# Optimization experiments

Hardware: AMD Instinct MI355X
Metric: run time of the kernel (lower is better)

## Reference

```python
import jax, jax.numpy as jnp
import numpy as np

B, N, D, H = 2, 512, 128, 8
DK = D // H

def setup_inputs() -> dict:
    key = jax.random.key(0)
    ks = jax.random.split(key, 7)
    s = lambda fan_in: 1.0 / np.sqrt(fan_in)
    return {
        "n": jax.random.normal(ks[0], (B, N, D), dtype=jnp.float32),
        "e": jax.random.normal(ks[1], (B, N, N, D), dtype=jnp.float32),
        "W_qkv": jax.random.normal(ks[2], (D, 3 * D), dtype=jnp.float32) * s(D),
        "O_n": jax.random.normal(ks[3], (D, D), dtype=jnp.float32) * s(D),
        "W_g": jax.random.normal(ks[4], (D, H), dtype=jnp.float32) * s(D),
        "W_e": jax.random.normal(ks[5], (D, H), dtype=jnp.float32) * s(D),
        "O_e": jax.random.normal(ks[6], (H, D), dtype=jnp.float32) * s(H),
    }

def reference(n, e, W_qkv, O_n, W_g, W_e, O_e):
    b, nn_, d = n.shape
    # QKV projection -> [B, H, N, DK] each
    qkv = (n @ W_qkv).reshape(b, nn_, 3, H, DK)
    qkv = jnp.transpose(qkv, (2, 0, 3, 1, 4))
    Q, K, V = qkv[0], qkv[1], qkv[2]
    # Edge bias and gate: [B, H, N, N]
    E = jnp.einsum('bnmd,dh->bhnm', e, W_e)
    G = jax.nn.sigmoid(jnp.einsum('bnmd,dh->bhnm', e, W_g))
    dyn_cent = jnp.log1p(G.sum(-1))  # [B, H, N]
    # Attention scores with clamp + edge bias
    A_raw = jnp.einsum('bhnd,bhmd->bhnm', Q, K) * (DK ** -0.5)
    A_raw = jnp.clip(A_raw, -5.0, 5.0)
    _E = A_raw + E
    A = jax.nn.softmax(_E, axis=-1)
    # Weighted values, rescaled by dynamic centrality
    _V = jnp.einsum('bhnm,bhmd->bhnd', A, V) * dyn_cent[..., None]
    n_out = jnp.transpose(_V, (0, 2, 1, 3)).reshape(b, nn_, d) @ O_n
    e_out = jnp.einsum('bhnm,hd->bnmd', _E, O_e)
    return n_out, e_out
```

## Files before the change

kernel.cpp:

```cpp
#include <hip/hip_runtime.h>
#include <math.h>

#define BB 2
#define NN 512
#define DD 128
#define HH 8
#define DKK 16
#define TR 128
#define NT (NN / TR)

typedef __attribute__((ext_vector_type(8))) short short8;
typedef __attribute__((ext_vector_type(4))) float f32x4;

__device__ __forceinline__ float dot4(float4 a, float4 b) {
    return a.x*b.x + a.y*b.y + a.z*b.z + a.w*b.w;
}
__device__ __forceinline__ unsigned pk_bf16(float a, float b) {
    unsigned ua = __float_as_uint(a), ub = __float_as_uint(b);
    ua = (ua + 0x7FFFu + ((ua >> 16) & 1u)) >> 16;
    ub = (ub + 0x7FFFu + ((ub >> 16) & 1u)) >> 16;
    return ua | (ub << 16);
}

__global__ __launch_bounds__(128)
void qkv_kernel(const float* __restrict__ n_in,
                const float* __restrict__ W_qkv,
                const float* __restrict__ W_g,
                const float* __restrict__ W_e,
                float* __restrict__ Qw, float* __restrict__ Kw,
                float* __restrict__ Vw, float* __restrict__ WegT)
{
    const int bid = blockIdx.x;
    if (bid >= BB * NN) {
        const int col = bid - BB * NN;
        const int t = threadIdx.x;
        WegT[col * DD + t] = (col < 8) ? W_e[t * HH + col]
                                       : W_g[t * HH + (col - 8)];
        return;
    }
    __shared__ float nrow[DD];
    const int bn = bid;
    const int b  = bn >> 9;
    const int nr = bn & 511;
    const int t  = threadIdx.x;
    nrow[t] = n_in[(size_t)bn * DD + t];
    __syncthreads();
    const int h = t >> 4, dk = t & 15;
    const size_t dst = ((size_t)(b * HH + h) * NN + nr) * DKK + dk;
    float accq = 0.f, acck = 0.f, accv = 0.f;
    #pragma unroll 8
    for (int d = 0; d < DD; ++d) {
        const float nv = nrow[d];
        const float* wr = W_qkv + (size_t)d * 3 * DD;
        accq += nv * wr[t];
        acck += nv * wr[t + 128];
        accv += nv * wr[t + 256];
    }
    Qw[dst] = accq;
    Kw[dst] = acck;
    Vw[dst] = accv;
}

__global__ __launch_bounds__(256)
void qk_kernel(const float* __restrict__ Qw,
               const float* __restrict__ Kw,
               float* __restrict__ QKc)
{
    __shared__ __align__(16) float4 Kl[NN * 4];
    __shared__ __align__(16) float4 Ql[32 * 4];

    const int bid = blockIdx.x;
    const int qt  = bid & 15;
    const int h   = (bid >> 4) & 7;
    const int b   = bid >> 7;
    const int t   = threadIdx.x;

    const float4* __restrict__ kb =
        (const float4*)Kw + ((size_t)(b * HH + h) * NN) * 4;
    #pragma unroll
    for (int j = 0; j < 8; ++j) Kl[j * 256 + t] = kb[j * 256 + t];
    if (t < 128)
        Ql[t] = ((const float4*)Qw)[((size_t)(b * HH + h) * NN + qt * 32) * 4 + t];
    __syncthreads();

    const int qr = t >> 3;
    const int mq = t & 7;
    const float4 q0 = Ql[qr * 4 + 0];
    const float4 q1 = Ql[qr * 4 + 1];
    const float4 q2 = Ql[qr * 4 + 2];
    const float4 q3 = Ql[qr * 4 + 3];

    float4* __restrict__ out4 =
        (float4*)QKc + (((size_t)(b * NN + qt * 32 + qr) * HH + h) * NN) / 4;

    #pragma unroll 1
    for (int c = 0; c < 16; ++c) {
        float4 r;
        float* rp = (float*)&r;
        #pragma unroll
        for (int i = 0; i < 4; ++i) {
            const int m = mq * 64 + c * 4 + i;
            float s = dot4(q0, Kl[m*4+0]) + dot4(q1, Kl[m*4+1])
                    + dot4(q2, Kl[m*4+2]) + dot4(q3, Kl[m*4+3]);
            s *= 0.25f;
            rp[i] = fminf(5.f, fmaxf(-5.f, s));
        }
        out4[mq * 16 + c] = r;
    }
}

__global__ __attribute__((amdgpu_flat_work_group_size(512, 512),
                          amdgpu_waves_per_eu(2, 4)))
void eg_kernel(const float* __restrict__ e,
               const float* __restrict__ WegT,
               const float* __restrict__ O_e,
               const float* __restrict__ QKc,
               const float* __restrict__ Vw,
               const float* __restrict__ O_n,
               float* __restrict__ n_out,
               float* __restrict__ e_out)
{
    __shared__ __align__(16) uint4 ebuf4[TR * 16];
    __shared__ __align__(16) float ET[HH * NN];
    __shared__ float Gred[64];
    __shared__ float dc[HH];
    __shared__ __align__(16) float vout[DD];

    const int t    = threadIdx.x;
    const int bn   = blockIdx.x;
    const int b    = bn >> 9;
    const int wq   = t >> 6;
    const int lane = t & 63;
    const int c    = lane & 15;
    const int mq   = lane >> 4;
    const int c4o  = t & 31;
    const int mr0  = t >> 5;

    const float4* __restrict__ e4    = (const float4*)e + (size_t)bn * NN * 32;
    const float4* __restrict__ WegT4 = (const float4*)WegT;

    short8 wB[4];
    #pragma unroll
    for (int kb = 0; kb < 4; ++kb) {
        const float4 wa = WegT4[c * 32 + kb * 8 + mq * 2];
        const float4 wb = WegT4[c * 32 + kb * 8 + mq * 2 + 1];
        uint4 u;
        u.x = pk_bf16(wa.x, wa.y); u.y = pk_bf16(wa.z, wa.w);
        u.z = pk_bf16(wb.x, wb.y); u.w = pk_bf16(wb.z, wb.w);
        wB[kb] = *(short8*)&u;
    }

    float4 pa0, pa1, pa2, pa3, pb0, pb1, pb2, pb3;

    #define STAGE_LOAD(tile)                                                  \
    {                                                                         \
        const float4* __restrict__ sp = e4 + (size_t)(tile) * 4096 + 2 * t;   \
        pa0 = sp[0];    pb0 = sp[1];                                          \
        pa1 = sp[1024]; pb1 = sp[1025];                                       \
        pa2 = sp[2048]; pb2 = sp[2049];                                       \
        pa3 = sp[3072]; pb3 = sp[3073];                                       \
    }
    #define STAGE_WRITE(P, A, B)                                              \
    {                                                                         \
        const int ms = (P) * 32 + (t >> 4), ck = t & 15;                      \
        uint4 u;                                                              \
        u.x = pk_bf16(A.x, A.y); u.y = pk_bf16(A.z, A.w);                     \
        u.z = pk_bf16(B.x, B.y); u.w = pk_bf16(B.z, B.w);                     \
        ebuf4[ms * 16 + (ck ^ (ms & 15))] = u;                                \
    }
    #define STAGE_WRITE_ALL()                                                 \
    {                                                                         \
        STAGE_WRITE(0, pa0, pb0); STAGE_WRITE(1, pa1, pb1);                   \
        STAGE_WRITE(2, pa2, pb2); STAGE_WRITE(3, pa3, pb3);                   \
    }

    float ga0 = 0.f, ga1 = 0.f, ga2 = 0.f, ga3 = 0.f;

    STAGE_LOAD(0);
    STAGE_WRITE_ALL();
    asm volatile("s_waitcnt lgkmcnt(0)" ::: "memory");
    __builtin_amdgcn_s_barrier();

    #pragma unroll
    for (int tt = 0; tt < NT; ++tt) {
        float4 qkv4 = {0.f, 0.f, 0.f, 0.f};
        if (c < 8)
            qkv4 = *(const float4*)(QKc + ((size_t)bn * HH + c) * NN
                                    + tt * TR + wq * 16 + mq * 4);
        if (tt + 1 < NT) STAGE_LOAD(tt + 1);

        const int mrow = wq * 16 + c;
        f32x4 acc = {0.f, 0.f, 0.f, 0.f};
        #pragma unroll
        for (int kb = 0; kb < 4; ++kb) {
            const int ck = kb * 4 + mq;
            uint4 av = ebuf4[mrow * 16 + (ck ^ (mrow & 15))];
            acc = __builtin_amdgcn_mfma_f32_16x16x32_bf16(
                      *(short8*)&av, wB[kb], acc, 0, 0, 0);
        }

        const int mloc = tt * TR + wq * 16 + mq * 4;
        if (c < 8) {
            ET[c * NN + mloc + 0] = acc[0] + qkv4.x;
            ET[c * NN + mloc + 1] = acc[1] + qkv4.y;
            ET[c * NN + mloc + 2] = acc[2] + qkv4.z;
            ET[c * NN + mloc + 3] = acc[3] + qkv4.w;
        } else {
            ga0 += 1.f / (1.f + __expf(-acc[0]));
            ga1 += 1.f / (1.f + __expf(-acc[1]));
            ga2 += 1.f / (1.f + __expf(-acc[2]));
            ga3 += 1.f / (1.f + __expf(-acc[3]));
        }
        asm volatile("s_waitcnt lgkmcnt(0)" ::: "memory");
        __builtin_amdgcn_s_barrier();

        if (tt + 1 < NT) {
            STAGE_WRITE_ALL();
            asm volatile("s_waitcnt lgkmcnt(0)" ::: "memory");
            __builtin_amdgcn_s_barrier();
        }
    }

    if (c >= 8) {
        float s = ga0 + ga1 + ga2 + ga3;
        s += __shfl_xor(s, 16, 64);
        s += __shfl_xor(s, 32, 64);
        if (lane < 16) Gred[wq * 8 + (c - 8)] = s;
    }
    __syncthreads();
    if (t < 8) {
        float s = 0.f;
        #pragma unroll
        for (int w = 0; w < 8; ++w) s += Gred[w * 8 + t];
        dc[t] = log1pf(s);
    }
    __syncthreads();

    {
        float4 oe[8];
        #pragma unroll
        for (int h = 0; h < 8; ++h)
            oe[h] = ((const float4*)O_e)[h * 32 + c4o];
        float4* __restrict__ out4 = (float4*)e_out + (size_t)bn * NN * 32;
        #pragma unroll 4
        for (int it = 0; it < 32; ++it) {
            const int m = mr0 + it * 16;
            float4 rr{0.f, 0.f, 0.f, 0.f};
            #pragma unroll
            for (int h = 0; h < 8; ++h) {
                const float ev = ET[h * NN + m];
                rr.x += ev * oe[h].x;
                rr.y += ev * oe[h].y;
                rr.z += ev * oe[h].z;
                rr.w += ev * oe[h].w;
            }
            out4[m * 32 + c4o] = rr;
        }
    }

    {
        const int h = wq;
        float vals[8];
        float rmax = -1e30f;
        #pragma unroll
        for (int k = 0; k < 8; ++k) {
            vals[k] = ET[h * NN + k * 64 + lane];
            rmax = fmaxf(rmax, vals[k]);
        }
        #pragma unroll
        for (int off = 32; off >= 1; off >>= 1)
            rmax = fmaxf(rmax, __shfl_xor(rmax, off, 64));
        float sum = 0.f;
        #pragma unroll
        for (int k = 0; k < 8; ++k) sum += __expf(vals[k] - rmax);
        #pragma unroll
        for (int off = 32; off >= 1; off >>= 1)
            sum += __shfl_xor(sum, off, 64);
        const float factor = dc[h] / sum;

        const int ddx = lane & 15, mg = lane >> 4;
        const float* __restrict__ vb = Vw + ((size_t)(b * HH + h) * NN) * DKK;
        float av = 0.f;
        #pragma unroll 4
        for (int m = mg; m < NN; m += 4) {
            const float p = __expf(ET[h * NN + m] - rmax);
            av += p * vb[m * DKK + ddx];
        }
        av += __shfl_xor(av, 16, 64);
        av += __shfl_xor(av, 32, 64);
        if (mg == 0) vout[h * DKK + ddx] = av * factor;
    }
    __syncthreads();

    if (t < DD) {
        float a3 = 0.f;
        #pragma unroll 4
        for (int d = 0; d < DD; ++d) a3 += vout[d] * O_n[d * DD + t];
        n_out[(size_t)bn * DD + t] = a3;
    }
    #undef STAGE_LOAD
    #undef STAGE_WRITE
    #undef STAGE_WRITE_ALL
}

extern "C" void kernel_launch(void* const* d_in, const int* in_sizes, int n_in,
                              void* d_out, int out_size, void* d_ws, size_t ws_size,
                              hipStream_t stream)
{
    const float* n_ptr = (const float*)d_in[0];
    const float* e     = (const float*)d_in[1];
    const float* W_qkv = (const float*)d_in[2];
    const float* O_n   = (const float*)d_in[3];
    const float* W_g   = (const float*)d_in[4];
    const float* W_e   = (const float*)d_in[5];
    const float* O_e   = (const float*)d_in[6];

    float* n_out = (float*)d_out;
    float* e_out = n_out + (size_t)BB * NN * DD;

    float* Qw   = (float*)d_ws;
    float* Kw   = Qw + (size_t)BB * HH * NN * DKK;
    float* Vw   = Kw + (size_t)BB * HH * NN * DKK;
    float* QKc  = Vw + (size_t)BB * HH * NN * DKK;
    float* WegT = QKc + (size_t)BB * HH * NN * NN;

    qkv_kernel<<<BB * NN + 16, 128, 0, stream>>>(n_ptr, W_qkv, W_g, W_e,
                                                 Qw, Kw, Vw, WegT);
    qk_kernel<<<BB * HH * 16, 256, 0, stream>>>(Qw, Kw, QKc);
    eg_kernel<<<BB * NN, 512, 0, stream>>>(e, WegT, O_e, QKc, Vw, O_n,
                                           n_out, e_out);
}
```

Baseline: 173.0 us.

## Fuse QK score computation into edge kernel, drop QKc intermediate buffer

Removes the separate qk_kernel and its 8 MB global QKc scratch buffer, which was written and then re-read by the edge kernel. Each eg_kernel block now computes its own row of clamped Q·K scores per head directly from global Q and K (K reads hit L2) into shared memory before the MFMA loop, which then accumulates the edge bias onto them in place. The ET stride is padded to 516 to reduce bank conflicts. In exchange, every block re-reads the full K for its batch and does the dot products redundantly with scalar FMAs.

```diff
diff --git a/kernel.cpp b/kernel.cpp
--- a/kernel.cpp
+++ b/kernel.cpp
@@ -8,6 +8,7 @@
 #define DKK 16
 #define TR 128
 #define NT (NN / TR)
+#define ETS 516
 
 typedef __attribute__((ext_vector_type(8))) short short8;
 typedef __attribute__((ext_vector_type(4))) float f32x4;
@@ -61,67 +62,20 @@
     Vw[dst] = accv;
 }
 
-__global__ __launch_bounds__(256)
-void qk_kernel(const float* __restrict__ Qw,
-               const float* __restrict__ Kw,
-               float* __restrict__ QKc)
-{
-    __shared__ __align__(16) float4 Kl[NN * 4];
-    __shared__ __align__(16) float4 Ql[32 * 4];
-
-    const int bid = blockIdx.x;
-    const int qt  = bid & 15;
-    const int h   = (bid >> 4) & 7;
-    const int b   = bid >> 7;
-    const int t   = threadIdx.x;
-
-    const float4* __restrict__ kb =
-        (const float4*)Kw + ((size_t)(b * HH + h) * NN) * 4;
-    #pragma unroll
-    for (int j = 0; j < 8; ++j) Kl[j * 256 + t] = kb[j * 256 + t];
-    if (t < 128)
-        Ql[t] = ((const float4*)Qw)[((size_t)(b * HH + h) * NN + qt * 32) * 4 + t];
-    __syncthreads();
-
-    const int qr = t >> 3;
-    const int mq = t & 7;
-    const float4 q0 = Ql[qr * 4 + 0];
-    const float4 q1 = Ql[qr * 4 + 1];
-    const float4 q2 = Ql[qr * 4 + 2];
-    const float4 q3 = Ql[qr * 4 + 3];
-
-    float4* __restrict__ out4 =
-        (float4*)QKc + (((size_t)(b * NN + qt * 32 + qr) * HH + h) * NN) / 4;
-
-    #pragma unroll 1
-    for (int c = 0; c < 16; ++c) {
-        float4 r;
-        float* rp = (float*)&r;
-        #pragma unroll
-        for (int i = 0; i < 4; ++i) {
-            const int m = mq * 64 + c * 4 + i;
-            float s = dot4(q0, Kl[m*4+0]) + dot4(q1, Kl[m*4+1])
-                    + dot4(q2, Kl[m*4+2]) + dot4(q3, Kl[m*4+3]);
-            s *= 0.25f;
-            rp[i] = fminf(5.f, fmaxf(-5.f, s));
-        }
-        out4[mq * 16 + c] = r;
-    }
-}
-
 __global__ __attribute__((amdgpu_flat_work_group_size(512, 512),
                           amdgpu_waves_per_eu(2, 4)))
 void eg_kernel(const float* __restrict__ e,
                const float* __restrict__ WegT,
                const float* __restrict__ O_e,
-               const float* __restrict__ QKc,
+               const float* __restrict__ Qw,
+               const float* __restrict__ Kw,
                const float* __restrict__ Vw,
                const float* __restrict__ O_n,
                float* __restrict__ n_out,
                float* __restrict__ e_out)
 {
     __shared__ __align__(16) uint4 ebuf4[TR * 16];
-    __shared__ __align__(16) float ET[HH * NN];
+    __shared__ __align__(16) float ET[HH * ETS];
     __shared__ float Gred[64];
     __shared__ float dc[HH];
     __shared__ __align__(16) float vout[DD];
@@ -129,6 +83,7 @@
     const int t    = threadIdx.x;
     const int bn   = blockIdx.x;
     const int b    = bn >> 9;
+    const int nr   = bn & 511;
     const int wq   = t >> 6;
     const int lane = t & 63;
     const int c    = lane & 15;
@@ -177,16 +132,30 @@
     float ga0 = 0.f, ga1 = 0.f, ga2 = 0.f, ga3 = 0.f;
 
     STAGE_LOAD(0);
+
+    {
+        const int h = wq;
+        const float4* __restrict__ qp =
+            (const float4*)(Qw + ((size_t)(b * HH + h) * NN + nr) * DKK);
+        const float4 q0 = qp[0], q1 = qp[1], q2 = qp[2], q3 = qp[3];
+        const float4* __restrict__ kb =
+            (const float4*)(Kw + ((size_t)(b * HH + h) * NN) * DKK);
+        #pragma unroll
+        for (int k = 0; k < 8; ++k) {
+            const int m = k * 64 + lane;
+            float s = dot4(q0, kb[m * 4 + 0]) + dot4(q1, kb[m * 4 + 1])
+                    + dot4(q2, kb[m * 4 + 2]) + dot4(q3, kb[m * 4 + 3]);
+            s *= 0.25f;
+            ET[h * ETS + m] = fminf(5.f, fmaxf(-5.f, s));
+        }
+    }
+
     STAGE_WRITE_ALL();
     asm volatile("s_waitcnt lgkmcnt(0)" ::: "memory");
     __builtin_amdgcn_s_barrier();
 
     #pragma unroll
     for (int tt = 0; tt < NT; ++tt) {
-        float4 qkv4 = {0.f, 0.f, 0.f, 0.f};
-        if (c < 8)
-            qkv4 = *(const float4*)(QKc + ((size_t)bn * HH + c) * NN
-                                    + tt * TR + wq * 16 + mq * 4);
         if (tt + 1 < NT) STAGE_LOAD(tt + 1);
 
         const int mrow = wq * 16 + c;
@@ -201,10 +170,10 @@
 
         const int mloc = tt * TR + wq * 16 + mq * 4;
         if (c < 8) {
-            ET[c * NN + mloc + 0] = acc[0] + qkv4.x;
-            ET[c * NN + mloc + 1] = acc[1] + qkv4.y;
-            ET[c * NN + mloc + 2] = acc[2] + qkv4.z;
-            ET[c * NN + mloc + 3] = acc[3] + qkv4.w;
+            float4 prev = *(float4*)&ET[c * ETS + mloc];
+            prev.x += acc[0]; prev.y += acc[1];
+            prev.z += acc[2]; prev.w += acc[3];
+            *(float4*)&ET[c * ETS + mloc] = prev;
         } else {
             ga0 += 1.f / (1.f + __expf(-acc[0]));
             ga1 += 1.f / (1.f + __expf(-acc[1]));
@@ -248,7 +217,7 @@
             float4 rr{0.f, 0.f, 0.f, 0.f};
             #pragma unroll
             for (int h = 0; h < 8; ++h) {
-                const float ev = ET[h * NN + m];
+                const float ev = ET[h * ETS + m];
                 rr.x += ev * oe[h].x;
                 rr.y += ev * oe[h].y;
                 rr.z += ev * oe[h].z;
@@ -264,7 +233,7 @@
         float rmax = -1e30f;
         #pragma unroll
         for (int k = 0; k < 8; ++k) {
-            vals[k] = ET[h * NN + k * 64 + lane];
+            vals[k] = ET[h * ETS + k * 64 + lane];
             rmax = fmaxf(rmax, vals[k]);
         }
         #pragma unroll
@@ -283,7 +252,7 @@
         float av = 0.f;
         #pragma unroll 4
         for (int m = mg; m < NN; m += 4) {
-            const float p = __expf(ET[h * NN + m] - rmax);
+            const float p = __expf(ET[h * ETS + m] - rmax);
             av += p * vb[m * DKK + ddx];
         }
         av += __shfl_xor(av, 16, 64);
@@ -321,12 +290,10 @@
     float* Qw   = (float*)d_ws;
     float* Kw   = Qw + (size_t)BB * HH * NN * DKK;
     float* Vw   = Kw + (size_t)BB * HH * NN * DKK;
-    float* QKc  = Vw + (size_t)BB * HH * NN * DKK;
-    float* WegT = QKc + (size_t)BB * HH * NN * NN;
+    float* WegT = Vw + (size_t)BB * HH * NN * DKK;
 
     qkv_kernel<<<BB * NN + 16, 128, 0, stream>>>(n_ptr, W_qkv, W_g, W_e,
                                                  Qw, Kw, Vw, WegT);
-    qk_kernel<<<BB * HH * 16, 256, 0, stream>>>(Qw, Kw, QKc);
-    eg_kernel<<<BB * NN, 512, 0, stream>>>(e, WegT, O_e, QKc, Vw, O_n,
+    eg_kernel<<<BB * NN, 512, 0, stream>>>(e, WegT, O_e, Qw, Kw, Vw, O_n,
                                            n_out, e_out);
 }
```

After: 156.0 us. -9.8%, faster.
